# Kernel optimization log

Hardware: AMD Instinct MI355X
Metric: run time of the kernel (lower is better)

Reference implementation:

```python
import jax, jax.numpy as jnp
import numpy as np

N_IN, N_HID, N_OUT, BATCH = 256, 1024, 256, 16384

def _lin(x, W, b=None):
    y = x @ W.T
    return y if b is None else y + b

def setup_inputs() -> dict:
    key = jax.random.key(0)
    ks = jax.random.split(key, 32)
    def xav(k, shape):
        fan_out, fan_in = shape
        lim = jnp.sqrt(6.0 / (fan_in + fan_out))
        return jax.random.uniform(k, shape, jnp.float32, -lim, lim)
    inp = {"x": jax.random.normal(ks[0], (BATCH, N_IN), jnp.float32)}
    # w0: torch code sets weight to ones, bias is default Linear init (uniform)
    inp["w0_w"] = jnp.ones((N_HID, N_IN), jnp.float32)
    inp["w0_b"] = jax.random.uniform(ks[1], (N_HID,), jnp.float32, -1/np.sqrt(N_IN), 1/np.sqrt(N_IN))
    i = 2
    for stage in (1, 2):
        for g in ("g", "z", "r", "h"):
            inp[f"u{g}{stage}"] = xav(ks[i], (N_HID, N_IN)); i += 1
            inp[f"w{g}{stage}_w"] = xav(ks[i], (N_HID, N_HID)); i += 1
            inp[f"w{g}{stage}_b"] = jax.random.uniform(ks[i], (N_HID,), jnp.float32, -1/np.sqrt(N_HID), 1/np.sqrt(N_HID)); i += 1
    inp["w4"] = xav(ks[i], (N_OUT, N_HID))
    return inp

def reference(x, w0_w, w0_b,
              ug1, wg1_w, wg1_b, uz1, wz1_w, wz1_b, ur1, wr1_w, wr1_b, uh1, wh1_w, wh1_b,
              ug2, wg2_w, wg2_b, uz2, wz2_w, wz2_b, ur2, wr2_w, wr2_b, uh2, wh2_w, wh2_b,
              w4):
    x = jnp.abs(x) + 0.1
    s0 = jnp.tanh(_lin(x, w0_w, w0_b))
    g1 = jnp.tanh(_lin(x, ug1) + _lin(s0, wg1_w, wg1_b))
    z1 = jnp.tanh(_lin(x, uz1) + _lin(s0, wz1_w, wz1_b))
    r1 = jnp.tanh(_lin(x, ur1) + _lin(s0, wr1_w, wr1_b))
    h1 = jnp.tanh(_lin(x, uh1) + _lin(s0 * r1, wh1_w, wh1_b))
    s1 = (1.0 - g1) * h1 + z1 * s0
    # NOTE: original computes stage-2 (g2,z2,r2,h2,s2) but returns w4(s1);
    # stage-2 is dead code and DCE'd by XLA, so it is omitted here.
    y = _lin(s1, w4)
    return y
```

## Files before the change

### kernel.cpp

```cpp
#include <hip/hip_runtime.h>
#include <hip/hip_bf16.h>
#include <stdint.h>


typedef unsigned short u16;
using f32x4  = __attribute__((ext_vector_type(4))) float;
using bf16x8 = __attribute__((ext_vector_type(8))) short;

#define BATCH 16384
#define NIN   256
#define NHID  1024
#define NOUT  256

#define BM 128
#define BN 128
#define BK2 64

__device__ __forceinline__ u16 f2bf(float f) {
  unsigned u = __builtin_bit_cast(unsigned, f);
  unsigned r = 0x7fffu + ((u >> 16) & 1u);
  return (u16)((u + r) >> 16);
}
__device__ __forceinline__ float bf2f(u16 h) {
  unsigned u = ((unsigned)h) << 16;
  return __builtin_bit_cast(float, u);
}
__device__ __forceinline__ float fast_tanh(float x) {
  float cx = fminf(fmaxf(x, -15.f), 15.f);
  float e  = __expf(2.f * cx);
  return (e - 1.f) / (e + 1.f);
}

__device__ __forceinline__ void gload_lds16(const u16* g, u16* l) {
  __builtin_amdgcn_global_load_lds(
      (__attribute__((address_space(1))) void*)(const_cast<u16*>(g)),
      (__attribute__((address_space(3))) void*)(l),
      16, 0, 0);
}

__device__ __forceinline__ void stage64(const u16* g0, int ld, u16* lds) {
  int t = threadIdx.x;
#pragma unroll
  for (int iss = 0; iss < 4; ++iss) {
    int idx = t + iss * 256;
    int row = idx >> 3;
    int j   = idx & 7;
    int c   = (j ^ (row & 7)) << 3;
    gload_lds16(g0 + (size_t)row * ld + c, lds + (size_t)idx * 8);
  }
}

__device__ __forceinline__ void mfma64(const u16* As, const u16* Bs,
                                       int wm, int wn, int lane,
                                       f32x4 acc[4][4]) {
  int r  = lane & 15;
  int q  = lane >> 4;
  int xr = r & 7;
#pragma unroll
  for (int ks = 0; ks < 2; ++ks) {
    int cx = ((ks * 4 + q) ^ xr) << 3;
    bf16x8 a[4], b[4];
#pragma unroll
    for (int i = 0; i < 4; ++i)
      a[i] = *(const bf16x8*)(As + (size_t)((wm + i * 16 + r) * BK2 + cx));
#pragma unroll
    for (int j = 0; j < 4; ++j)
      b[j] = *(const bf16x8*)(Bs + (size_t)((wn + j * 16 + r) * BK2 + cx));
#pragma unroll
    for (int i = 0; i < 4; ++i)
#pragma unroll
      for (int j = 0; j < 4; ++j)
        acc[i][j] = __builtin_amdgcn_mfma_f32_16x16x32_bf16(a[i], b[j], acc[i][j], 0, 0, 0);
  }
}

__device__ __forceinline__ void pipe_step(const u16* At, int lda,
                                          const u16* Bt, int ldb,
                                          int t, int STEPS,
                                          u16* Ac, u16* Bc, u16* An, u16* Bn,
                                          int wm, int wn, int lane,
                                          f32x4 acc[4][4]) {
  if (t + 1 < STEPS) {
    stage64(At + (size_t)(t + 1) * BK2, lda, An);
    stage64(Bt + (size_t)(t + 1) * BK2, ldb, Bn);
    asm volatile("s_waitcnt vmcnt(8)" ::: "memory");
  } else {
    asm volatile("s_waitcnt vmcnt(0)" ::: "memory");
  }
  __builtin_amdgcn_s_barrier();
  mfma64(Ac, Bc, wm, wn, lane, acc);
  asm volatile("s_waitcnt lgkmcnt(0)" ::: "memory");
  __builtin_amdgcn_s_barrier();
}

template<int STEPS>
__device__ __forceinline__ void gemm_pipe(const u16* A, int lda,
                                          const u16* B, int ldb,
                                          int m0, int n0, u16* sm,
                                          int wm, int wn, int lane,
                                          f32x4 acc[4][4]) {
  const u16* At = A + (size_t)m0 * lda;
  const u16* Bt = B + (size_t)n0 * ldb;
  u16* As0 = sm;          u16* Bs0 = sm + 8192;
  u16* As1 = sm + 16384;  u16* Bs1 = sm + 24576;
  stage64(At, lda, As0);
  stage64(Bt, ldb, Bs0);
  static_assert(STEPS % 2 == 0, "even steps");
#pragma unroll
  for (int tt = 0; tt < STEPS / 2; ++tt) {
    pipe_step(At, lda, Bt, ldb, 2 * tt,     STEPS, As0, Bs0, As1, Bs1, wm, wn, lane, acc);
    pipe_step(At, lda, Bt, ldb, 2 * tt + 1, STEPS, As1, Bs1, As0, Bs0, wm, wn, lane, acc);
  }
}

__device__ __forceinline__ void zero_acc(f32x4 acc[4][4]) {
  f32x4 z = {0.f, 0.f, 0.f, 0.f};
#pragma unroll
  for (int i = 0; i < 4; ++i)
#pragma unroll
    for (int j = 0; j < 4; ++j) acc[i][j] = z;
}


struct Prep {
  const float* x; u16* xa;
  const float* csrc[6]; u16* cdst[6]; int cblk[6];
  const float* w[3]; const float* bb[3]; float* c[3];
};

__global__ __launch_bounds__(256) void k_prep(Prep P) {
  int b = blockIdx.x;
  if (b < 4096) {
    int i = b * 256 + threadIdx.x;
    float4 v = ((const float4*)P.x)[i];
    ushort4 o;
    o.x = f2bf(fabsf(v.x) + 0.1f);
    o.y = f2bf(fabsf(v.y) + 0.1f);
    o.z = f2bf(fabsf(v.z) + 0.1f);
    o.w = f2bf(fabsf(v.w) + 0.1f);
    ((ushort4*)P.xa)[i] = o;
  } else if (b < 6400) {
    int rb = b - 4096;
    int k = 0;
#pragma unroll
    for (int t = 0; t < 5; ++t)
      if (rb >= P.cblk[k]) { rb -= P.cblk[k]; ++k; }
    int i = rb * 256 + threadIdx.x;
    float4 v = ((const float4*)P.csrc[k])[i];
    ushort4 o;
    o.x = f2bf(v.x); o.y = f2bf(v.y); o.z = f2bf(v.z); o.w = f2bf(v.w);
    ((ushort4*)P.cdst[k])[i] = o;
  } else {
    int rb = b - 6400;
    int g = rb >> 10, n = rb & 1023;
    const float* row = P.w[g] + (size_t)n * NHID;
    float s = 0.f;
    for (int k = threadIdx.x; k < NHID; k += 256) s += row[k];
#pragma unroll
    for (int o = 32; o; o >>= 1) s += __shfl_down(s, o, 64);
    __shared__ float sm[4];
    if ((threadIdx.x & 63) == 0) sm[threadIdx.x >> 6] = s;
    __syncthreads();
    if (threadIdx.x == 0) P.c[g][n] = sm[0] + sm[1] + sm[2] + sm[3] + P.bb[g][n];
  }
}


__global__ __launch_bounds__(256) void k_pass_r(const u16* __restrict__ xa,
                                                const u16* __restrict__ ur,
                                                const float* __restrict__ cr,
                                                u16* __restrict__ r1) {
  __shared__ __align__(16) u16 smem[32768];
  int m0 = blockIdx.y * BM, n0 = blockIdx.x * BN;
  int lane = threadIdx.x & 63, wave = threadIdx.x >> 6;
  int wm = (wave >> 1) * 64, wn = (wave & 1) * 64;
  f32x4 acc[4][4];
  zero_acc(acc);
  gemm_pipe<4>(xa, NIN, ur, NIN, m0, n0, smem, wm, wn, lane, acc);

  int crw = (lane >> 4) * 4, cc = lane & 15;
#pragma unroll
  for (int ni = 0; ni < 4; ++ni) {
    int col = n0 + wn + ni * 16 + cc;
    float bias = cr[col];
#pragma unroll
    for (int mi = 0; mi < 4; ++mi)
#pragma unroll
      for (int r = 0; r < 4; ++r) {
        int row = m0 + wm + mi * 16 + crw + r;
        r1[(size_t)row * NHID + col] = f2bf(fast_tanh(acc[mi][ni][r] + bias));
      }
  }
}

__global__ __launch_bounds__(256) void k_gates_h(
    const u16* __restrict__ xa,
    const u16* __restrict__ ug, const u16* __restrict__ uz,
    const u16* __restrict__ uh,
    const float* __restrict__ cg, const float* __restrict__ cz,
    const float* __restrict__ bh,
    const u16* __restrict__ r1, const u16* __restrict__ wh,
    u16* __restrict__ s1) {
  __shared__ __align__(16) u16 smem[32768];

  int wg  = blockIdx.x;
  int xcd = wg & 7;
  int idx = wg >> 3;
  int mb  = xcd * 16 + (idx >> 3);
  int nb  = idx & 7;
  int m0 = mb * BM, n0 = nb * BN;

  int lane = threadIdx.x & 63, wave = threadIdx.x >> 6;
  int wm = (wave >> 1) * 64, wn = (wave & 1) * 64;
  int crw = (lane >> 4) * 4, cc = lane & 15;

  f32x4 acc[4][4];
  unsigned pg[4][4][2], pz[4][4][2];

  zero_acc(acc);
  gemm_pipe<4>(xa, NIN, ug, NIN, m0, n0, smem, wm, wn, lane, acc);
#pragma unroll
  for (int ni = 0; ni < 4; ++ni) {
    float cv = cg[n0 + wn + ni * 16 + cc];
#pragma unroll
    for (int mi = 0; mi < 4; ++mi) {
      float v0 = 1.f - fast_tanh(acc[mi][ni][0] + cv);
      float v1 = 1.f - fast_tanh(acc[mi][ni][1] + cv);
      float v2 = 1.f - fast_tanh(acc[mi][ni][2] + cv);
      float v3 = 1.f - fast_tanh(acc[mi][ni][3] + cv);
      pg[mi][ni][0] = (unsigned)f2bf(v0) | ((unsigned)f2bf(v1) << 16);
      pg[mi][ni][1] = (unsigned)f2bf(v2) | ((unsigned)f2bf(v3) << 16);
    }
  }

  zero_acc(acc);
  gemm_pipe<4>(xa, NIN, uz, NIN, m0, n0, smem, wm, wn, lane, acc);
#pragma unroll
  for (int ni = 0; ni < 4; ++ni) {
    float cv = cz[n0 + wn + ni * 16 + cc];
#pragma unroll
    for (int mi = 0; mi < 4; ++mi) {
      float v0 = fast_tanh(acc[mi][ni][0] + cv);
      float v1 = fast_tanh(acc[mi][ni][1] + cv);
      float v2 = fast_tanh(acc[mi][ni][2] + cv);
      float v3 = fast_tanh(acc[mi][ni][3] + cv);
      pz[mi][ni][0] = (unsigned)f2bf(v0) | ((unsigned)f2bf(v1) << 16);
      pz[mi][ni][1] = (unsigned)f2bf(v2) | ((unsigned)f2bf(v3) << 16);
    }
  }

  zero_acc(acc);
  gemm_pipe<4>(xa, NIN, uh, NIN, m0, n0, smem, wm, wn, lane, acc);
  gemm_pipe<16>(r1, NHID, wh, NHID, m0, n0, smem, wm, wn, lane, acc);

#pragma unroll
  for (int ni = 0; ni < 4; ++ni) {
    int col = n0 + wn + ni * 16 + cc;
    float bias = bh[col];
#pragma unroll
    for (int mi = 0; mi < 4; ++mi)
#pragma unroll
      for (int r = 0; r < 4; ++r) {
        int row = m0 + wm + mi * 16 + crw + r;
        float h = fast_tanh(acc[mi][ni][r] + bias);
        unsigned pgw = pg[mi][ni][r >> 1];
        unsigned pzw = pz[mi][ni][r >> 1];
        u16 pgh = (r & 1) ? (u16)(pgw >> 16) : (u16)(pgw & 0xffff);
        u16 pzh = (r & 1) ? (u16)(pzw >> 16) : (u16)(pzw & 0xffff);
        float s = bf2f(pgh) * h + bf2f(pzh);
        s1[(size_t)row * NHID + col] = f2bf(s);
      }
  }
}

__global__ __launch_bounds__(256) void k_pass_c(const u16* __restrict__ s1,
                                                const u16* __restrict__ w4,
                                                float* __restrict__ y) {
  __shared__ __align__(16) u16 smem[32768];
  int m0 = blockIdx.y * BM, n0 = blockIdx.x * BN;
  int lane = threadIdx.x & 63, wave = threadIdx.x >> 6;
  int wm = (wave >> 1) * 64, wn = (wave & 1) * 64;
  f32x4 acc[4][4];
  zero_acc(acc);
  gemm_pipe<16>(s1, NHID, w4, NHID, m0, n0, smem, wm, wn, lane, acc);

  int crw = (lane >> 4) * 4, cc = lane & 15;
#pragma unroll
  for (int ni = 0; ni < 4; ++ni) {
    int col = n0 + wn + ni * 16 + cc;
#pragma unroll
    for (int mi = 0; mi < 4; ++mi)
#pragma unroll
      for (int r = 0; r < 4; ++r) {
        int row = m0 + wm + mi * 16 + crw + r;
        y[(size_t)row * NOUT + col] = acc[mi][ni][r];
      }
  }
}


extern "C" void kernel_launch(void* const* d_in, const int* in_sizes, int n_in,
                              void* d_out, int out_size, void* d_ws, size_t ws_size,
                              hipStream_t stream) {
  (void)in_sizes; (void)n_in; (void)out_size; (void)ws_size;

  const float* x    = (const float*)d_in[0];
  const float* ug1  = (const float*)d_in[3];
  const float* wg1w = (const float*)d_in[4];
  const float* wg1b = (const float*)d_in[5];
  const float* uz1  = (const float*)d_in[6];
  const float* wz1w = (const float*)d_in[7];
  const float* wz1b = (const float*)d_in[8];
  const float* ur1  = (const float*)d_in[9];
  const float* wr1w = (const float*)d_in[10];
  const float* wr1b = (const float*)d_in[11];
  const float* uh1  = (const float*)d_in[12];
  const float* wh1w = (const float*)d_in[13];
  const float* wh1b = (const float*)d_in[14];
  const float* w4   = (const float*)d_in[27];
  float* y = (float*)d_out;

  uint8_t* ws = (uint8_t*)d_ws;
  size_t off = 0;
  auto carve = [&](size_t bytes) -> void* {
    void* p = ws + off;
    off += (bytes + 255) & ~(size_t)255;
    return p;
  };
  u16* xa  = (u16*)carve((size_t)BATCH * NIN * 2);
  u16* r1  = (u16*)carve((size_t)BATCH * NHID * 2);
  u16* s1  = (u16*)carve((size_t)BATCH * NHID * 2);
  u16* bug = (u16*)carve((size_t)NHID * NIN * 2);
  u16* buz = (u16*)carve((size_t)NHID * NIN * 2);
  u16* bur = (u16*)carve((size_t)NHID * NIN * 2);
  u16* buh = (u16*)carve((size_t)NHID * NIN * 2);
  u16* bwh = (u16*)carve((size_t)NHID * NHID * 2);
  u16* bw4 = (u16*)carve((size_t)NOUT * NHID * 2);
  float* cg = (float*)carve(NHID * 4);
  float* cz = (float*)carve(NHID * 4);
  float* cr = (float*)carve(NHID * 4);

  Prep P;
  P.x = x; P.xa = xa;
  P.csrc[0] = ug1;  P.cdst[0] = bug; P.cblk[0] = 256;
  P.csrc[1] = uz1;  P.cdst[1] = buz; P.cblk[1] = 256;
  P.csrc[2] = ur1;  P.cdst[2] = bur; P.cblk[2] = 256;
  P.csrc[3] = uh1;  P.cdst[3] = buh; P.cblk[3] = 256;
  P.csrc[4] = wh1w; P.cdst[4] = bwh; P.cblk[4] = 1024;
  P.csrc[5] = w4;   P.cdst[5] = bw4; P.cblk[5] = 256;
  P.w[0] = wg1w; P.bb[0] = wg1b; P.c[0] = cg;
  P.w[1] = wz1w; P.bb[1] = wz1b; P.c[1] = cz;
  P.w[2] = wr1w; P.bb[2] = wr1b; P.c[2] = cr;
  k_prep<<<9472, 256, 0, stream>>>(P);

  k_pass_r<<<dim3(NHID / BN, BATCH / BM), 256, 0, stream>>>(xa, bur, cr, r1);

  k_gates_h<<<(NHID / BN) * (BATCH / BM), 256, 0, stream>>>(
      xa, bug, buz, buh, cg, cz, wh1b, r1, bwh, s1);

  k_pass_c<<<dim3(NOUT / BN, BATCH / BM), 256, 0, stream>>>(s1, bw4, y);
}
```

Baseline: 153.9 us.

## Enlarge gates_h tile to 256x128 with 512-thread blocks and 96KB LDS

Replaces k_gates_h with a 512-thread variant in which each block computes a 256x128 output tile using eight waves. New staging helpers and a single-buffer-pair pipeline keep double-buffered A and B tiles in 96KB of dynamic LDS. Each B (weight) tile is now reused across twice as many rows, which cuts global and L2 traffic per MFMA and halves the block count. The cost is one block per CU with large LDS use. It also depends on the launch being allowed more than 64KB of dynamic shared memory.

Measured after the change: 143.4 us. 6.9% less time.

```diff
diff --git a/kernel.cpp b/kernel.cpp
--- a/kernel.cpp
+++ b/kernel.cpp
@@ -37,6 +37,7 @@
       (__attribute__((address_space(3))) void*)(l),
       16, 0, 0);
 }
+
 
 __device__ __forceinline__ void stage64(const u16* g0, int ld, u16* lds) {
   int t = threadIdx.x;
@@ -119,6 +120,65 @@
   for (int i = 0; i < 4; ++i)
 #pragma unroll
     for (int j = 0; j < 4; ++j) acc[i][j] = z;
+}
+
+
+__device__ __forceinline__ void stageA8(const u16* g0, int ld, u16* lds) {
+  int t = threadIdx.x;
+#pragma unroll
+  for (int iss = 0; iss < 4; ++iss) {
+    int idx = t + iss * 512;
+    int row = idx >> 3;
+    int j   = idx & 7;
+    int c   = (j ^ (row & 7)) << 3;
+    gload_lds16(g0 + (size_t)row * ld + c, lds + (size_t)idx * 8);
+  }
+}
+__device__ __forceinline__ void stageB8(const u16* g0, int ld, u16* lds) {
+  int t = threadIdx.x;
+#pragma unroll
+  for (int iss = 0; iss < 2; ++iss) {
+    int idx = t + iss * 512;
+    int row = idx >> 3;
+    int j   = idx & 7;
+    int c   = (j ^ (row & 7)) << 3;
+    gload_lds16(g0 + (size_t)row * ld + c, lds + (size_t)idx * 8);
+  }
+}
+
+__device__ __forceinline__ void pipe_step8(const u16* At, int lda,
+                                           const u16* Bt, int ldb,
+                                           int t, int STEPS, u16* sm,
+                                           int wm, int wn, int lane,
+                                           f32x4 acc[4][4]) {
+  if (t + 1 < STEPS) {
+    u16* nb = sm + (size_t)((t + 1) & 1) * 24576;
+    stageA8(At + (size_t)(t + 1) * BK2, lda, nb);
+    stageB8(Bt + (size_t)(t + 1) * BK2, ldb, nb + 16384);
+    asm volatile("s_waitcnt vmcnt(6)" ::: "memory");
+  } else {
+    asm volatile("s_waitcnt vmcnt(0)" ::: "memory");
+  }
+  __builtin_amdgcn_s_barrier();
+  u16* cur = sm + (size_t)(t & 1) * 24576;
+  mfma64(cur, cur + 16384, wm, wn, lane, acc);
+  asm volatile("s_waitcnt lgkmcnt(0)" ::: "memory");
+  __builtin_amdgcn_s_barrier();
+}
+
+template<int STEPS>
+__device__ __forceinline__ void gemm_pipe8(const u16* A, int lda,
+                                           const u16* B, int ldb,
+                                           int m0, int n0, u16* sm,
+                                           int wm, int wn, int lane,
+                                           f32x4 acc[4][4]) {
+  const u16* At = A + (size_t)m0 * lda;
+  const u16* Bt = B + (size_t)n0 * ldb;
+  stageA8(At, lda, sm);
+  stageB8(Bt, ldb, sm + 16384);
+#pragma unroll
+  for (int t = 0; t < STEPS; ++t)
+    pipe_step8(At, lda, Bt, ldb, t, STEPS, sm, wm, wn, lane, acc);
 }
 
 
@@ -193,7 +253,7 @@
   }
 }
 
-__global__ __launch_bounds__(256) void k_gates_h(
+__global__ __launch_bounds__(512, 1) void k_gates_h512(
     const u16* __restrict__ xa,
     const u16* __restrict__ ug, const u16* __restrict__ uz,
     const u16* __restrict__ uh,
@@ -201,24 +261,25 @@
     const float* __restrict__ bh,
     const u16* __restrict__ r1, const u16* __restrict__ wh,
     u16* __restrict__ s1) {
-  __shared__ __align__(16) u16 smem[32768];
-
-  int wg  = blockIdx.x;
-  int xcd = wg & 7;
-  int idx = wg >> 3;
-  int mb  = xcd * 16 + (idx >> 3);
+  extern __shared__ __align__(16) u16 smem[];
+
+  int bid = blockIdx.x;
+  int xcd = bid & 7;
+  int idx = bid >> 3;
+  int mb  = xcd * 8 + (idx >> 3);
   int nb  = idx & 7;
-  int m0 = mb * BM, n0 = nb * BN;
+  int m0 = mb * 256, n0 = nb * 128;
 
   int lane = threadIdx.x & 63, wave = threadIdx.x >> 6;
-  int wm = (wave >> 1) * 64, wn = (wave & 1) * 64;
+  int wm = (wave >> 1) * 64;
+  int wn = (wave & 1) * 64;
   int crw = (lane >> 4) * 4, cc = lane & 15;
 
   f32x4 acc[4][4];
   unsigned pg[4][4][2], pz[4][4][2];
 
   zero_acc(acc);
-  gemm_pipe<4>(xa, NIN, ug, NIN, m0, n0, smem, wm, wn, lane, acc);
+  gemm_pipe8<4>(xa, NIN, ug, NIN, m0, n0, smem, wm, wn, lane, acc);
 #pragma unroll
   for (int ni = 0; ni < 4; ++ni) {
     float cv = cg[n0 + wn + ni * 16 + cc];
@@ -234,7 +295,7 @@
   }
 
   zero_acc(acc);
-  gemm_pipe<4>(xa, NIN, uz, NIN, m0, n0, smem, wm, wn, lane, acc);
+  gemm_pipe8<4>(xa, NIN, uz, NIN, m0, n0, smem, wm, wn, lane, acc);
 #pragma unroll
   for (int ni = 0; ni < 4; ++ni) {
     float cv = cz[n0 + wn + ni * 16 + cc];
@@ -250,8 +311,8 @@
   }
 
   zero_acc(acc);
-  gemm_pipe<4>(xa, NIN, uh, NIN, m0, n0, smem, wm, wn, lane, acc);
-  gemm_pipe<16>(r1, NHID, wh, NHID, m0, n0, smem, wm, wn, lane, acc);
+  gemm_pipe8<4>(xa, NIN, uh, NIN, m0, n0, smem, wm, wn, lane, acc);
+  gemm_pipe8<16>(r1, NHID, wh, NHID, m0, n0, smem, wm, wn, lane, acc);
 
 #pragma unroll
   for (int ni = 0; ni < 4; ++ni) {
@@ -355,7 +416,7 @@
 
   k_pass_r<<<dim3(NHID / BN, BATCH / BM), 256, 0, stream>>>(xa, bur, cr, r1);
 
-  k_gates_h<<<(NHID / BN) * (BATCH / BM), 256, 0, stream>>>(
+  k_gates_h512<<<(BATCH / 256) * (NHID / 128), 512, 98304, stream>>>(
       xa, bug, buz, buh, cg, cz, wh1b, r1, bwh, s1);
 
   k_pass_c<<<dim3(NOUT / BN, BATCH / BM), 256, 0, stream>>>(s1, bw4, y);
```
